# Kernel optimization log

Measured on AMD Instinct MI355X. Metric: run time of the kernel, lower is better.

The kernel has to match this reference:

```python
import jax, jax.numpy as jnp
import numpy as np

B, P, K, H = 8, 4096, 20, 128  # graphs, points per graph, kNN, hidden_channels


def _linear_init(key, fin, fout):
    s = 1.0 / np.sqrt(fin)
    kw, kb = jax.random.split(key)
    W = jax.random.uniform(kw, (fin, fout), jnp.float32, -s, s)
    b = jax.random.uniform(kb, (fout,), jnp.float32, -s, s)
    return W, b


def setup_inputs() -> dict:
    key = jax.random.key(0)
    ks = jax.random.split(key, 6)
    x = jax.random.normal(ks[0], (B, P, 3), jnp.float32)
    W1, b1 = _linear_init(ks[1], 2 * 3, H)
    W2, b2 = _linear_init(ks[2], 2 * H, H)
    W3, b3 = _linear_init(ks[3], 2 * H, H)
    W4, b4 = _linear_init(ks[4], H, H)
    W5, b5 = _linear_init(ks[5], H, 3)
    return dict(x=x, W1=W1, b1=b1, W2=W2, b2=b2, W3=W3, b3=b3,
                W4=W4, b4=b4, W5=W5, b5=b5)


def _dynamic_edge_conv(x, W, b):
    # x: [B, P, D]. Recompute kNN graph in feature space, EdgeConv with max aggr.
    sq = jnp.sum(x * x, axis=-1)                                   # [B, P]
    d2 = sq[:, :, None] + sq[:, None, :] - 2.0 * jnp.einsum('bid,bjd->bij', x, x)
    eye = jnp.eye(x.shape[1], dtype=bool)                          # exclude self-loops
    d2 = jnp.where(eye[None], jnp.inf, d2)
    _, idx = jax.lax.top_k(-d2, K)                                 # [B, P, K]
    xj = jax.vmap(lambda xb, ib: xb[ib])(x, idx)                   # [B, P, K, D] gather
    xi = jnp.broadcast_to(x[:, :, None, :], xj.shape)
    e = jnp.concatenate([xi, xj - xi], axis=-1)                    # [B, P, K, 2D]
    h = jax.nn.relu(e @ W + b)                                     # edge MLP
    return jnp.max(h, axis=2)                                      # max aggregation -> [B, P, H]


def reference(x, W1, b1, W2, b2, W3, b3, W4, b4, W5, b5):
    h = jax.nn.relu(_dynamic_edge_conv(x, W1, b1))
    h = jax.nn.relu(_dynamic_edge_conv(h, W2, b2))
    h = jax.nn.relu(_dynamic_edge_conv(h, W3, b3))
    g = jnp.mean(h, axis=1)                                        # global_mean_pool -> [B, H]
    g = jax.nn.relu(g @ W4 + b4)
    # dropout is identity in eval mode
    return g @ W5 + b5                                             # [B, 3]
```

## Files before the change

kernel.cpp:

```cpp
#include <hip/hip_runtime.h>
#include <hip/hip_bf16.h>


static constexpr int B_ = 8, P_ = 4096, K_ = 20, H_ = 128;
static constexpr float FINF = 3.0e38f;
static constexpr int CAPH = 160;

typedef __attribute__((ext_vector_type(8))) short short8;
typedef __attribute__((ext_vector_type(16))) float floatx16;

__device__ __forceinline__ float dist3(float x0, float x1, float x2,
                                       const float4& v) {
  return fmaf(-2.f, fmaf(x0, v.x, fmaf(x1, v.y, x2 * v.z)), v.w);
}

__global__ __launch_bounds__(256) void pack4_kernel(const float* __restrict__ X,
                                                    float4* __restrict__ pt4) {
  int p = blockIdx.x * 256 + threadIdx.x;
  const float* row = X + (size_t)p * 3;
  float4 v;
  v.x = row[0]; v.y = row[1]; v.z = row[2];
  v.w = fmaf(v.x, v.x, fmaf(v.y, v.y, v.z * v.z));
  pt4[p] = v;
}

__global__ __launch_bounds__(256) void split_kernel(const float* __restrict__ X,
                                                    ushort* __restrict__ hi,
                                                    ushort* __restrict__ lo,
                                                    float* __restrict__ sqn) {
  int t = blockIdx.x * 256 + threadIdx.x;
  int gp = t >> 4;
  int q = t & 15;
  const float* src = X + ((size_t)gp << 7) + (q << 3);
  size_t dst = ((size_t)gp << 7) + ((size_t)(q ^ (gp & 15)) << 3);
  float4 v0 = *(const float4*)src;
  float4 v1 = *(const float4*)(src + 4);
  float vv[8] = {v0.x, v0.y, v0.z, v0.w, v1.x, v1.y, v1.z, v1.w};
  ushort h[8], l[8];
  float ss = 0.f;
#pragma unroll
  for (int e = 0; e < 8; ++e) {
    ss = fmaf(vv[e], vv[e], ss);
    __hip_bfloat16 hb = __float2bfloat16(vv[e]);
    float hf = __bfloat162float(hb);
    __hip_bfloat16 lb = __float2bfloat16(vv[e] - hf);
    h[e] = *(ushort*)&hb;
    l[e] = *(ushort*)&lb;
  }
  *(short8*)(hi + dst) = *(short8*)h;
  *(short8*)(lo + dst) = *(short8*)l;
#pragma unroll
  for (int off = 1; off < 16; off <<= 1) ss += __shfl_xor(ss, off);
  if (q == 0) sqn[gp] = ss;
}

__global__ __launch_bounds__(256) void feat3_kernel(
    const float* __restrict__ X, const float* __restrict__ W,
    const float* __restrict__ bias, float* __restrict__ c_out,
    float* __restrict__ u_out) {
  const int h = threadIdx.x & (H_ - 1);
  const int pg = threadIdx.x >> 7;
  const int bb = blockIdx.x & 7;
  const int pb = blockIdx.x >> 3;
  const int p0 = bb * P_ + pb * 8 + pg * 4;
  float a0 = 0, a1 = 0, a2 = 0, a3 = 0, u0 = 0, u1 = 0, u2 = 0, u3 = 0;
  const float* xp = X + (size_t)p0 * 3;
#pragma unroll
  for (int d = 0; d < 3; ++d) {
    float wt = W[d * H_ + h];
    float wb = W[(3 + d) * H_ + h];
    float x0 = xp[d], x1 = xp[3 + d], x2 = xp[6 + d], x3 = xp[9 + d];
    a0 = fmaf(x0, wt, a0); u0 = fmaf(x0, wb, u0);
    a1 = fmaf(x1, wt, a1); u1 = fmaf(x1, wb, u1);
    a2 = fmaf(x2, wt, a2); u2 = fmaf(x2, wb, u2);
    a3 = fmaf(x3, wt, a3); u3 = fmaf(x3, wb, u3);
  }
  float bv = bias[h];
  c_out[(size_t)(p0 + 0) * H_ + h] = a0 - u0 + bv;
  c_out[(size_t)(p0 + 1) * H_ + h] = a1 - u1 + bv;
  c_out[(size_t)(p0 + 2) * H_ + h] = a2 - u2 + bv;
  c_out[(size_t)(p0 + 3) * H_ + h] = a3 - u3 + bv;
  u_out[(size_t)(p0 + 0) * H_ + h] = u0;
  u_out[(size_t)(p0 + 1) * H_ + h] = u1;
  u_out[(size_t)(p0 + 2) * H_ + h] = u2;
  u_out[(size_t)(p0 + 3) * H_ + h] = u3;
}

__global__ __launch_bounds__(256) void wprep_kernel(const float* __restrict__ W,
                                                    ushort* __restrict__ Vfh,
                                                    ushort* __restrict__ Vfl) {
  int tid = blockIdx.x * 256 + threadIdx.x;
  int t = tid >> 9;
  int s = (tid >> 6) & 7;
  int lane = tid & 63;
  int col = t * 32 + (lane & 31);
  int kb = s * 16 + ((lane >> 5) << 3);
  ushort h[8], l[8];
#pragma unroll
  for (int e = 0; e < 8; ++e) {
    int k = kb + e;
    float v;
    if (col < 128) v = W[k * H_ + col] - W[(128 + k) * H_ + col];
    else v = W[(128 + k) * H_ + col - 128];
    __hip_bfloat16 hb = __float2bfloat16(v);
    float hf = __bfloat162float(hb);
    __hip_bfloat16 lb = __float2bfloat16(v - hf);
    h[e] = *(ushort*)&hb;
    l[e] = *(ushort*)&lb;
  }
  size_t off = (size_t)((t * 8 + s) * 64 + lane) * 8;
  *(short8*)(Vfh + off) = *(short8*)h;
  *(short8*)(Vfl + off) = *(short8*)l;
}

__device__ __forceinline__ void stage_async(const ushort* __restrict__ Xhi,
                                            const ushort* __restrict__ Xlo,
                                            size_t tile, char* buf, int w,
                                            int lane) {
  const char* gh = (const char*)(Xhi + tile);
  const char* gl = (const char*)(Xlo + tile);
  const int lo16 = lane * 16;
#pragma unroll
  for (int it = 0; it < 4; ++it) {
    const int off = (w * 4 + it) * 1024;
    __builtin_amdgcn_global_load_lds(
        (const __attribute__((address_space(1))) void*)(gh + off + lo16),
        (__attribute__((address_space(3))) void*)(buf + off), 16, 0, 0);
    __builtin_amdgcn_global_load_lds(
        (const __attribute__((address_space(1))) void*)(gl + off + lo16),
        (__attribute__((address_space(3))) void*)(buf + 16384 + off), 16, 0, 0);
  }
}

__device__ __forceinline__ void stage_async32(const ushort* __restrict__ Xhi,
                                              const ushort* __restrict__ Xlo,
                                              size_t tile, char* buf, int w,
                                              int lane) {
  const char* gh = (const char*)(Xhi + tile);
  const char* gl = (const char*)(Xlo + tile);
  const int lo16 = lane * 16;
#pragma unroll
  for (int it = 0; it < 4; ++it) {
    const int off = (w * 4 + it) * 1024;
    __builtin_amdgcn_global_load_lds(
        (const __attribute__((address_space(1))) void*)(gh + off + lo16),
        (__attribute__((address_space(3))) void*)(buf + off), 16, 0, 0);
    __builtin_amdgcn_global_load_lds(
        (const __attribute__((address_space(1))) void*)(gl + off + lo16),
        (__attribute__((address_space(3))) void*)(buf + 8192 + off), 16, 0, 0);
  }
}

__device__ __forceinline__ void load_afrag_sw(const ushort* __restrict__ X,
                                              size_t gb, int row, int lane,
                                              short8* a) {
  const ushort* base = X + (gb + row) * (size_t)H_;
  const int x = row & 15;
  const int kh = lane >> 5;
#pragma unroll
  for (int s = 0; s < 8; ++s) {
    a[s] = *(const short8*)(base + (((s * 2 + kh) ^ x) << 3));
  }
}

__device__ __forceinline__ floatx16 gram32(const char* lds, const short8* ahi,
                                           const short8* alo, int jh,
                                           int lane) {
  floatx16 a0, a1, a2;
#pragma unroll
  for (int i = 0; i < 16; ++i) { a0[i] = 0.f; a1[i] = 0.f; a2[i] = 0.f; }
  const int base = (jh * 32 + (lane & 31)) * 256;
  const int kh = lane >> 5;
  const int x = lane & 15;
#pragma unroll
  for (int s = 0; s < 8; ++s) {
    const int off = base + (((s * 2 + kh) ^ x) << 4);
    short8 bh = *(const short8*)(lds + off);
    short8 bl = *(const short8*)(lds + 16384 + off);
    a0 = __builtin_amdgcn_mfma_f32_32x32x16_bf16(ahi[s], bh, a0, 0, 0, 0);
    a1 = __builtin_amdgcn_mfma_f32_32x32x16_bf16(ahi[s], bl, a1, 0, 0, 0);
    a2 = __builtin_amdgcn_mfma_f32_32x32x16_bf16(alo[s], bh, a2, 0, 0, 0);
  }
  floatx16 acc;
#pragma unroll
  for (int i = 0; i < 16; ++i) acc[i] = (a0[i] + a1[i]) + a2[i];
  return acc;
}

__device__ __forceinline__ floatx16 gram32t(const char* lds, const short8* ahi,
                                            const short8* alo, int lane) {
  floatx16 a0, a1, a2;
#pragma unroll
  for (int i = 0; i < 16; ++i) { a0[i] = 0.f; a1[i] = 0.f; a2[i] = 0.f; }
  const int base = (lane & 31) * 256;
  const int kh = lane >> 5;
  const int x = lane & 15;
#pragma unroll
  for (int s = 0; s < 8; ++s) {
    const int off = base + (((s * 2 + kh) ^ x) << 4);
    short8 bh = *(const short8*)(lds + off);
    short8 bl = *(const short8*)(lds + 8192 + off);
    a0 = __builtin_amdgcn_mfma_f32_32x32x16_bf16(ahi[s], bh, a0, 0, 0, 0);
    a1 = __builtin_amdgcn_mfma_f32_32x32x16_bf16(ahi[s], bl, a1, 0, 0, 0);
    a2 = __builtin_amdgcn_mfma_f32_32x32x16_bf16(alo[s], bh, a2, 0, 0, 0);
  }
  floatx16 acc;
#pragma unroll
  for (int i = 0; i < 16; ++i) acc[i] = (a0[i] + a1[i]) + a2[i];
  return acc;
}

__global__ __launch_bounds__(256) void feat_mfma_kernel(
    const ushort* __restrict__ Xhi, const ushort* __restrict__ Xlo,
    const ushort* __restrict__ Vfh, const ushort* __restrict__ Vfl,
    const float* __restrict__ bias, float* __restrict__ c_out,
    float* __restrict__ u_out) {
  const int lane = threadIdx.x & 63;
  const int w = threadIdx.x >> 6;
  const int b = blockIdx.x & 7;
  const int i0 = (blockIdx.x >> 3) * 32;
  const size_t gb = (size_t)b * P_;

  short8 ahi[8], alo[8];
  const int arow = i0 + (lane & 31);
  load_afrag_sw(Xhi, gb, arow, lane, ahi);
  load_afrag_sw(Xlo, gb, arow, lane, alo);

  const int rl = 4 * (lane >> 5);
#pragma unroll
  for (int tt = 0; tt < 2; ++tt) {
    const int t = w * 2 + tt;
    floatx16 a0, a1, a2;
#pragma unroll
    for (int i = 0; i < 16; ++i) { a0[i] = 0.f; a1[i] = 0.f; a2[i] = 0.f; }
#pragma unroll
    for (int s = 0; s < 8; ++s) {
      const size_t off = (size_t)((t * 8 + s) * 64 + lane) * 8;
      short8 bh = *(const short8*)(Vfh + off);
      short8 bl = *(const short8*)(Vfl + off);
      a0 = __builtin_amdgcn_mfma_f32_32x32x16_bf16(ahi[s], bh, a0, 0, 0, 0);
      a1 = __builtin_amdgcn_mfma_f32_32x32x16_bf16(ahi[s], bl, a1, 0, 0, 0);
      a2 = __builtin_amdgcn_mfma_f32_32x32x16_bf16(alo[s], bh, a2, 0, 0, 0);
    }
    const int col = t * 32 + (lane & 31);
    if (t < 4) {
      float bv = bias[col];
#pragma unroll
      for (int g = 0; g < 16; ++g) {
        int row = i0 + rl + (g & 3) + 8 * (g >> 2);
        c_out[(gb + row) * (size_t)H_ + col] = ((a0[g] + a1[g]) + a2[g]) + bv;
      }
    } else {
#pragma unroll
      for (int g = 0; g < 16; ++g) {
        int row = i0 + rl + (g & 3) + 8 * (g >> 2);
        u_out[(gb + row) * (size_t)H_ + col - 128] = (a0[g] + a1[g]) + a2[g];
      }
    }
  }
}

__device__ __forceinline__ float kth20_of32(float* v) {
  float m = 0.f;
  for (int sel = 0; sel < K_; ++sel) {
    m = v[0];
#pragma unroll
    for (int t = 1; t < 32; ++t) m = fminf(m, v[t]);
    bool done = false;
#pragma unroll
    for (int t = 0; t < 32; ++t) {
      if (!done && v[t] == m) { v[t] = FINF; done = true; }
    }
  }
  return m;
}

__global__ __launch_bounds__(256) void knn_part_kernel(
    const ushort* __restrict__ Xhi, const ushort* __restrict__ Xlo,
    const float* __restrict__ sqn, float* __restrict__ tau) {
  __shared__ char buf[32768];
  __shared__ float ldist[64 * 65];

  const int tid = threadIdx.x;
  const int lane = tid & 63;
  const int w = tid >> 6;
  const int rh = w >> 1, jh = w & 1;
  const int b = blockIdx.x & 7;
  const int i0 = (blockIdx.x >> 3) * 64;
  const size_t gb = (size_t)b * P_;

  short8 ahi[8], alo[8];
  const int arow = i0 + rh * 32 + (lane & 31);
  load_afrag_sw(Xhi, gb, arow, lane, ahi);
  load_afrag_sw(Xlo, gb, arow, lane, alo);
  const int rowb = rh * 32 + 4 * (lane >> 5);
  const int jcol = jh * 32 + (lane & 31);

  const int srow = tid >> 2;
  const int sr = tid & 3;
  const int gi = i0 + srow;
  float bd[8];
#pragma unroll
  for (int k = 0; k < 8; ++k) bd[k] = FINF;
  float worst = FINF;

  for (int ch = 0; ch < 8; ++ch) {
    const int tb = ch * 64;
    stage_async(Xhi, Xlo, (gb + tb) * (size_t)H_, buf, w, lane);
    float sqv = sqn[gb + tb + jcol];
    __syncthreads();
    floatx16 acc = gram32(buf, ahi, alo, jh, lane);
#pragma unroll
    for (int g = 0; g < 16; ++g) {
      ldist[(rowb + (g & 3) + 8 * (g >> 2)) * 65 + jcol] =
          fmaf(-2.f, acc[g], sqv);
    }
    __syncthreads();
    const float* drow = ldist + srow * 65 + sr * 16;
#pragma unroll 4
    for (int jj = 0; jj < 16; ++jj) {
      float s = drow[jj];
      int jg = tb + sr * 16 + jj;
      if (s < worst && jg != gi) {
        bool done = false;
#pragma unroll
        for (int k = 0; k < 8; ++k) {
          if (!done && bd[k] == worst) { bd[k] = s; done = true; }
        }
        worst = bd[0];
#pragma unroll
        for (int k = 1; k < 8; ++k) worst = fmaxf(worst, bd[k]);
      }
    }
  }
  __syncthreads();
#pragma unroll
  for (int k = 0; k < 8; ++k) ldist[srow * 65 + sr * 8 + k] = bd[k];
  __syncthreads();
  if (sr == 0) {
    float v[32];
#pragma unroll
    for (int t = 0; t < 32; ++t) v[t] = ldist[srow * 65 + t];
    tau[gb + gi] = kth20_of32(v);
  }
}

__global__ __launch_bounds__(128) void knn_compact_kernel(
    const ushort* __restrict__ Xhi, const ushort* __restrict__ Xlo,
    const float* __restrict__ sqn, const float* __restrict__ tau,
    float2* __restrict__ cand, int* __restrict__ cnt) {
  __shared__ char buf[2][16384];

  const int tid = threadIdx.x;
  const int lane = tid & 63;
  const int w = tid >> 6;
  const int b = blockIdx.x & 7;
  const int rest = blockIdx.x >> 3;
  const int half = rest & 1;
  const int i0 = (rest >> 1) * 64;
  const size_t gb = (size_t)b * P_;

  short8 ahi[8], alo[8];
  const int arow = i0 + w * 32 + (lane & 31);
  load_afrag_sw(Xhi, gb, arow, lane, ahi);
  load_afrag_sw(Xlo, gb, arow, lane, alo);

  const int rowb = i0 + w * 32 + 4 * (lane >> 5);
  float taur[16];
  int cur[16];
#pragma unroll
  for (int g = 0; g < 16; ++g) {
    taur[g] = tau[gb + rowb + (g & 3) + 8 * (g >> 2)];
    cur[g] = 0;
  }
  float2* candrow = cand + (gb + rowb) * (size_t)(2 * CAPH) + half * CAPH;
  const unsigned lmask = (1u << (lane & 31)) - 1u;
  const int jbase = half * 2048;

  stage_async32(Xhi, Xlo, (gb + jbase) * (size_t)H_, buf[0], w, lane);
  float sqv_next = sqn[gb + jbase + (lane & 31)];

  for (int c = 0; c < 64; ++c) {
    const int tb = jbase + c * 32;
    __syncthreads();
    float sqv = sqv_next;
    if (c < 63) {
      stage_async32(Xhi, Xlo, (gb + tb + 32) * (size_t)H_, buf[(c + 1) & 1], w,
                    lane);
      sqv_next = sqn[gb + tb + 32 + (lane & 31)];
    }
    floatx16 acc = gram32t(buf[c & 1], ahi, alo, lane);
    const int jg = tb + (lane & 31);
#pragma unroll
    for (int g = 0; g < 16; ++g) {
      float d = fmaf(-2.f, acc[g], sqv);
      bool pred = (d <= taur[g]);
      unsigned long long mk = __ballot(pred);
      if (mk) {
        unsigned seg = (lane >= 32) ? (unsigned)(mk >> 32) : (unsigned)mk;
        int idx = cur[g] + __popc(seg & lmask);
        if (pred && idx < CAPH) {
          float2 e;
          e.x = d;
          e.y = __int_as_float(jg);
          candrow[(size_t)((g & 3) + 8 * (g >> 2)) * (2 * CAPH) + idx] = e;
        }
        cur[g] += __popc(seg);
      }
    }
  }
  if ((lane & 31) == 0) {
#pragma unroll
    for (int g = 0; g < 16; ++g) {
      int row = rowb + (g & 3) + 8 * (g >> 2);
      cnt[(gb + row) * 2 + half] = cur[g] < CAPH ? cur[g] : CAPH;
    }
  }
}

__global__ __launch_bounds__(256) void knn3_part_kernel(
    const float4* __restrict__ pt4, float* __restrict__ tau) {
  __shared__ float lv[64 * 33];
  const int tid = threadIdx.x;
  const int row_local = tid >> 2;
  const int r = tid & 3;
  const int b = blockIdx.x & 7;
  const int i0 = (blockIdx.x >> 3) * 64;
  const int gi = i0 + row_local;
  const size_t gb = (size_t)b * P_;

  float4 pi = pt4[gb + gi];
  float bd[8];
#pragma unroll
  for (int k = 0; k < 8; ++k) bd[k] = FINF;
  float worst = FINF;

  const float4* pg = pt4 + gb + r * 256;
#pragma unroll 4
  for (int jj = 0; jj < 256; ++jj) {
    float4 v = pg[jj];
    float d = dist3(pi.x, pi.y, pi.z, v);
    int jg = r * 256 + jj;
    if (d < worst && jg != gi) {
      bool done = false;
#pragma unroll
      for (int k = 0; k < 8; ++k) {
        if (!done && bd[k] == worst) { bd[k] = d; done = true; }
      }
      worst = bd[0];
#pragma unroll
      for (int k = 1; k < 8; ++k) worst = fmaxf(worst, bd[k]);
    }
  }
#pragma unroll
  for (int k = 0; k < 8; ++k) lv[row_local * 33 + r * 8 + k] = bd[k];
  __syncthreads();
  if (r == 0) {
    float v[32];
#pragma unroll
    for (int t = 0; t < 32; ++t) v[t] = lv[row_local * 33 + t];
    tau[gb + gi] = kth20_of32(v);
  }
}

__global__ __launch_bounds__(256) void knn3_compact_kernel(
    const float4* __restrict__ pt4, const float* __restrict__ tau,
    float2* __restrict__ cand, int* __restrict__ cnt) {
  const int tid = threadIdx.x;
  const int lane = tid & 63;
  const int w = tid >> 6;
  const int b = blockIdx.x & 7;
  const int rest = blockIdx.x >> 3;
  const int half = rest & 1;
  const int i0 = (rest >> 1) * 64;
  const size_t gb = (size_t)b * P_;
  const int r0 = i0 + w * 16;

  float xr0[16], xr1[16], xr2[16], taur[16];
  int cur[16];
#pragma unroll
  for (int r = 0; r < 16; ++r) {
    float4 p = pt4[gb + r0 + r];
    xr0[r] = p.x; xr1[r] = p.y; xr2[r] = p.z;
    taur[r] = tau[gb + r0 + r];
    cur[r] = 0;
  }

  const float4* pg = pt4 + gb + half * 2048;
  for (int ch = 0; ch < 32; ++ch) {
    float4 v = pg[ch * 64 + lane];
    int jg = half * 2048 + ch * 64 + lane;
#pragma unroll
    for (int r = 0; r < 16; ++r) {
      float d = dist3(xr0[r], xr1[r], xr2[r], v);
      bool pred = (d <= taur[r]);
      unsigned long long mk = __ballot(pred);
      if (mk) {
        int n = __popcll(mk);
        int pre = __popcll(mk & ((1ull << lane) - 1ull));
        int idx = cur[r] + pre;
        if (pred && idx < CAPH) {
          float2 e;
          e.x = d;
          e.y = __int_as_float(jg);
          cand[(gb + r0 + r) * (size_t)(2 * CAPH) + half * CAPH + idx] = e;
        }
        cur[r] += n;
      }
    }
  }
  if (lane == 0) {
#pragma unroll
    for (int r = 0; r < 16; ++r)
      cnt[(gb + r0 + r) * 2 + half] = cur[r] < CAPH ? cur[r] : CAPH;
  }
}

__global__ __launch_bounds__(256) void select_aggr_kernel(
    const float2* __restrict__ cand, const int* __restrict__ cnt,
    const float* __restrict__ c, const float* __restrict__ u,
    float* __restrict__ out) {
  __shared__ int ljs[4][24];
  const int w = threadIdx.x >> 6;
  const int lane = threadIdx.x & 63;
  const int b = blockIdx.x & 7;
  const int row = b * P_ + (blockIdx.x >> 3) * 4 + w;
  const int c0 = cnt[row * 2], c1 = cnt[row * 2 + 1];
  const int ctot = c0 + c1;
  float d[5];
  int j[5];
#pragma unroll
  for (int s = 0; s < 5; ++s) {
    int m = s * 64 + lane;
    bool valid = m < ctot;
    int addr = (m < c0) ? m : (CAPH + m - c0);
    if (!valid) addr = 0;
    float2 e = cand[(size_t)row * (2 * CAPH) + addr];
    d[s] = valid ? e.x : FINF;
    j[s] = __float_as_int(e.y);
  }
  for (int round = 0; round < K_ + 1; ++round) {
    float bm = d[0];
    int bs = 0;
#pragma unroll
    for (int s = 1; s < 5; ++s) {
      if (d[s] < bm) { bm = d[s]; bs = s; }
    }
    int id = (lane << 3) | bs;
#pragma unroll
    for (int off = 1; off < 64; off <<= 1) {
      float od = __shfl_xor(bm, off);
      int oid = __shfl_xor(id, off);
      if (od < bm || (od == bm && oid < id)) { bm = od; id = oid; }
    }
    int owner = id >> 3, os = id & 7;
    if (lane == owner) {
      int jv = 0;
#pragma unroll
      for (int s = 0; s < 5; ++s) {
        if (s == os) { jv = j[s]; d[s] = FINF; }
      }
      ljs[w][round] = jv;
    }
  }
  const float2* c2p = (const float2*)(c + (size_t)row * H_);
  float2 ci = c2p[lane];
  float mx = 0.f, my = 0.f;
#pragma unroll 4
  for (int k = 1; k <= K_; ++k) {
    int jj = ljs[w][k];
    float2 uv = *(const float2*)(u + ((size_t)(b << 12) + jj) * H_ + lane * 2);
    mx = fmaxf(mx, ci.x + uv.x);
    my = fmaxf(my, ci.y + uv.y);
  }
  float2 o;
  o.x = mx; o.y = my;
  *(float2*)(out + (size_t)row * H_ + lane * 2) = o;
}

__global__ __launch_bounds__(128) void pool_kernel(const float* __restrict__ hf,
                                                   float* __restrict__ psum) {
  constexpr int CHUNK = 64;
  int blk = blockIdx.x;
  int b = blk >> 6;
  int chunk = blk & 63;
  int h = threadIdx.x;
  int base = (b << 12) + chunk * CHUNK;
  float acc = 0.f;
#pragma unroll 4
  for (int p = 0; p < CHUNK; ++p) acc += hf[(size_t)(base + p) * H_ + h];
  psum[blk * H_ + h] = acc;
}

__global__ __launch_bounds__(128) void head_kernel(
    const float* __restrict__ psum, const float* __restrict__ W4,
    const float* __restrict__ b4, const float* __restrict__ W5,
    const float* __restrict__ b5, float* __restrict__ out) {
  int b = blockIdx.x, h = threadIdx.x;
  __shared__ float g[H_];
  __shared__ float t[H_];
  float s = 0.f;
#pragma unroll 4
  for (int ch = 0; ch < 64; ++ch) s += psum[(b * 64 + ch) * H_ + h];
  g[h] = s * (1.0f / P_);
  __syncthreads();
  float acc = b4[h];
#pragma unroll 4
  for (int d = 0; d < H_; ++d) acc = fmaf(g[d], W4[d * H_ + h], acc);
  t[h] = fmaxf(acc, 0.f);
  __syncthreads();
  if (h < 3) {
    float o = b5[h];
#pragma unroll 4
    for (int d = 0; d < H_; ++d) o = fmaf(t[d], W5[d * 3 + h], o);
    out[b * 3 + h] = o;
  }
}

extern "C" void kernel_launch(void* const* d_in, const int* in_sizes, int n_in,
                              void* d_out, int out_size, void* d_ws,
                              size_t ws_size, hipStream_t stream) {
  const float* x  = (const float*)d_in[0];
  const float* W1 = (const float*)d_in[1];
  const float* b1 = (const float*)d_in[2];
  const float* W2 = (const float*)d_in[3];
  const float* b2 = (const float*)d_in[4];
  const float* W3 = (const float*)d_in[5];
  const float* b3 = (const float*)d_in[6];
  const float* W4 = (const float*)d_in[7];
  const float* b4 = (const float*)d_in[8];
  const float* W5 = (const float*)d_in[9];
  const float* b5 = (const float*)d_in[10];
  float* out = (float*)d_out;

  char* ws = (char*)d_ws;
  const size_t NF = (size_t)B_ * P_ * H_;
  const size_t NP_ = (size_t)B_ * P_;
  float*  bufA = (float*)ws;  ws += NF * 4;
  float*  bufB = (float*)ws;  ws += NF * 4;
  float*  bufU = (float*)ws;  ws += NF * 4;
  ushort* xhi  = (ushort*)ws; ws += NF * 2;
  ushort* xlo  = (ushort*)ws; ws += NF * 2;
  float*  sqn  = (float*)ws;  ws += NP_ * 4;
  float*  psum = (float*)ws;  ws += (size_t)B_ * 64 * H_ * 4;
  float*  tau  = (float*)ws;  ws += NP_ * 4;
  int*    cnt  = (int*)ws;    ws += NP_ * 2 * 4;
  float4* pt4  = (float4*)ws; ws += NP_ * 16;
  ushort* vfh  = (ushort*)ws; ws += 32768 * 2;
  ushort* vfl  = (ushort*)ws; ws += 32768 * 2;
  float2* cand = (float2*)ws; ws += NP_ * (size_t)(2 * CAPH) * 8;

  const int NP = B_ * P_;
  dim3 blk256(256), blk128(128);

  pack4_kernel<<<NP / 256, blk256, 0, stream>>>(x, pt4);
  feat3_kernel<<<NP / 8, blk256, 0, stream>>>(x, W1, b1, bufA, bufU);
  knn3_part_kernel<<<B_ * 64, blk256, 0, stream>>>(pt4, tau);
  knn3_compact_kernel<<<B_ * 64 * 2, blk256, 0, stream>>>(pt4, tau, cand, cnt);
  select_aggr_kernel<<<NP / 4, blk256, 0, stream>>>(cand, cnt, bufA, bufU, bufA);

  split_kernel<<<(int)(NF / 8 / 256), blk256, 0, stream>>>(bufA, xhi, xlo, sqn);
  wprep_kernel<<<16, blk256, 0, stream>>>(W2, vfh, vfl);
  feat_mfma_kernel<<<NP / 32, blk256, 0, stream>>>(xhi, xlo, vfh, vfl, b2, bufB, bufU);
  knn_part_kernel<<<B_ * 64, blk256, 0, stream>>>(xhi, xlo, sqn, tau);
  knn_compact_kernel<<<B_ * 64 * 2, blk128, 0, stream>>>(xhi, xlo, sqn, tau, cand, cnt);
  select_aggr_kernel<<<NP / 4, blk256, 0, stream>>>(cand, cnt, bufB, bufU, bufB);

  split_kernel<<<(int)(NF / 8 / 256), blk256, 0, stream>>>(bufB, xhi, xlo, sqn);
  wprep_kernel<<<16, blk256, 0, stream>>>(W3, vfh, vfl);
  feat_mfma_kernel<<<NP / 32, blk256, 0, stream>>>(xhi, xlo, vfh, vfl, b3, bufA, bufU);
  knn_part_kernel<<<B_ * 64, blk256, 0, stream>>>(xhi, xlo, sqn, tau);
  knn_compact_kernel<<<B_ * 64 * 2, blk128, 0, stream>>>(xhi, xlo, sqn, tau, cand, cnt);
  select_aggr_kernel<<<NP / 4, blk256, 0, stream>>>(cand, cnt, bufA, bufU, bufA);

  pool_kernel<<<B_ * 64, blk128, 0, stream>>>(bufA, psum);
  head_kernel<<<B_, blk128, 0, stream>>>(psum, W4, b4, W5, b5, out);
}
```

Baseline: 1.104 ms.

## Fuse kernels across layers to cut launches and intermediate traffic

Merges several stages into fewer kernels. pack4 moves into the first feature kernel, the two wprep launches become one, and the layer-1 kNN part and compact steps become one kernel with tau kept in LDS. The bf16 hi/lo split and squared norms move into the aggregation epilogue, and the MFMA feature GEMM moves into the kNN-part kernel, which now handles 64 rows per block. This removes kernel launches and a full read and write of the fp32 activations per layer. In exchange, the fused kNN kernel recomputes the partial top-k in each of its two halves, and the feature GEMM now runs on fewer, larger blocks.

```diff
diff --git a/kernel.cpp b/kernel.cpp
--- a/kernel.cpp
+++ b/kernel.cpp
@@ -14,55 +14,31 @@
   return fmaf(-2.f, fmaf(x0, v.x, fmaf(x1, v.y, x2 * v.z)), v.w);
 }
 
-__global__ __launch_bounds__(256) void pack4_kernel(const float* __restrict__ X,
-                                                    float4* __restrict__ pt4) {
-  int p = blockIdx.x * 256 + threadIdx.x;
-  const float* row = X + (size_t)p * 3;
-  float4 v;
-  v.x = row[0]; v.y = row[1]; v.z = row[2];
-  v.w = fmaf(v.x, v.x, fmaf(v.y, v.y, v.z * v.z));
-  pt4[p] = v;
-}
-
-__global__ __launch_bounds__(256) void split_kernel(const float* __restrict__ X,
-                                                    ushort* __restrict__ hi,
-                                                    ushort* __restrict__ lo,
-                                                    float* __restrict__ sqn) {
-  int t = blockIdx.x * 256 + threadIdx.x;
-  int gp = t >> 4;
-  int q = t & 15;
-  const float* src = X + ((size_t)gp << 7) + (q << 3);
-  size_t dst = ((size_t)gp << 7) + ((size_t)(q ^ (gp & 15)) << 3);
-  float4 v0 = *(const float4*)src;
-  float4 v1 = *(const float4*)(src + 4);
-  float vv[8] = {v0.x, v0.y, v0.z, v0.w, v1.x, v1.y, v1.z, v1.w};
-  ushort h[8], l[8];
-  float ss = 0.f;
-#pragma unroll
-  for (int e = 0; e < 8; ++e) {
-    ss = fmaf(vv[e], vv[e], ss);
-    __hip_bfloat16 hb = __float2bfloat16(vv[e]);
-    float hf = __bfloat162float(hb);
-    __hip_bfloat16 lb = __float2bfloat16(vv[e] - hf);
-    h[e] = *(ushort*)&hb;
-    l[e] = *(ushort*)&lb;
-  }
-  *(short8*)(hi + dst) = *(short8*)h;
-  *(short8*)(lo + dst) = *(short8*)l;
-#pragma unroll
-  for (int off = 1; off < 16; off <<= 1) ss += __shfl_xor(ss, off);
-  if (q == 0) sqn[gp] = ss;
-}
-
-__global__ __launch_bounds__(256) void feat3_kernel(
+__device__ __forceinline__ void cvt_split(float v, ushort& h, ushort& l) {
+  __hip_bfloat16 hb = __float2bfloat16(v);
+  float hf = __bfloat162float(hb);
+  __hip_bfloat16 lb = __float2bfloat16(v - hf);
+  h = *(ushort*)&hb;
+  l = *(ushort*)&lb;
+}
+
+__global__ __launch_bounds__(256) void feat3p_kernel(
     const float* __restrict__ X, const float* __restrict__ W,
     const float* __restrict__ bias, float* __restrict__ c_out,
-    float* __restrict__ u_out) {
+    float* __restrict__ u_out, float4* __restrict__ pt4) {
   const int h = threadIdx.x & (H_ - 1);
   const int pg = threadIdx.x >> 7;
   const int bb = blockIdx.x & 7;
   const int pb = blockIdx.x >> 3;
-  const int p0 = bb * P_ + pb * 8 + pg * 4;
+  const int pbase = bb * P_ + pb * 8;
+  const int p0 = pbase + pg * 4;
+  if (threadIdx.x < 8) {
+    const float* row = X + (size_t)(pbase + threadIdx.x) * 3;
+    float4 v;
+    v.x = row[0]; v.y = row[1]; v.z = row[2];
+    v.w = fmaf(v.x, v.x, fmaf(v.y, v.y, v.z * v.z));
+    pt4[pbase + threadIdx.x] = v;
+  }
   float a0 = 0, a1 = 0, a2 = 0, a3 = 0, u0 = 0, u1 = 0, u2 = 0, u3 = 0;
   const float* xp = X + (size_t)p0 * 3;
 #pragma unroll
@@ -86,10 +62,15 @@
   u_out[(size_t)(p0 + 3) * H_ + h] = u3;
 }
 
-__global__ __launch_bounds__(256) void wprep_kernel(const float* __restrict__ W,
-                                                    ushort* __restrict__ Vfh,
-                                                    ushort* __restrict__ Vfl) {
-  int tid = blockIdx.x * 256 + threadIdx.x;
+__global__ __launch_bounds__(256) void wprep2_kernel(
+    const float* __restrict__ W2, const float* __restrict__ W3,
+    ushort* __restrict__ Vfh2, ushort* __restrict__ Vfl2,
+    ushort* __restrict__ Vfh3, ushort* __restrict__ Vfl3) {
+  const int which = blockIdx.x >> 4;
+  const float* W = which ? W3 : W2;
+  ushort* Vfh = which ? Vfh3 : Vfh2;
+  ushort* Vfl = which ? Vfl3 : Vfl2;
+  int tid = (blockIdx.x & 15) * 256 + threadIdx.x;
   int t = tid >> 9;
   int s = (tid >> 6) & 7;
   int lane = tid & 63;
@@ -102,11 +83,7 @@
     float v;
     if (col < 128) v = W[k * H_ + col] - W[(128 + k) * H_ + col];
     else v = W[(128 + k) * H_ + col - 128];
-    __hip_bfloat16 hb = __float2bfloat16(v);
-    float hf = __bfloat162float(hb);
-    __hip_bfloat16 lb = __float2bfloat16(v - hf);
-    h[e] = *(ushort*)&hb;
-    l[e] = *(ushort*)&lb;
+    cvt_split(v, h[e], l[e]);
   }
   size_t off = (size_t)((t * 8 + s) * 64 + lane) * 8;
   *(short8*)(Vfh + off) = *(short8*)h;
@@ -210,26 +187,47 @@
   return acc;
 }
 
-__global__ __launch_bounds__(256) void feat_mfma_kernel(
+__device__ __forceinline__ float kth20_of32(float* v) {
+  float m = 0.f;
+  for (int sel = 0; sel < K_; ++sel) {
+    m = v[0];
+#pragma unroll
+    for (int t = 1; t < 32; ++t) m = fminf(m, v[t]);
+    bool done = false;
+#pragma unroll
+    for (int t = 0; t < 32; ++t) {
+      if (!done && v[t] == m) { v[t] = FINF; done = true; }
+    }
+  }
+  return m;
+}
+
+__global__ __launch_bounds__(256) void featpart_kernel(
     const ushort* __restrict__ Xhi, const ushort* __restrict__ Xlo,
     const ushort* __restrict__ Vfh, const ushort* __restrict__ Vfl,
     const float* __restrict__ bias, float* __restrict__ c_out,
-    float* __restrict__ u_out) {
-  const int lane = threadIdx.x & 63;
-  const int w = threadIdx.x >> 6;
+    float* __restrict__ u_out, const float* __restrict__ sqn,
+    float* __restrict__ tau) {
+  __shared__ char buf[32768];
+  __shared__ float ldist[64 * 65];
+
+  const int tid = threadIdx.x;
+  const int lane = tid & 63;
+  const int w = tid >> 6;
+  const int rh = w >> 1, jh = w & 1;
   const int b = blockIdx.x & 7;
-  const int i0 = (blockIdx.x >> 3) * 32;
+  const int i0 = (blockIdx.x >> 3) * 64;
   const size_t gb = (size_t)b * P_;
 
   short8 ahi[8], alo[8];
-  const int arow = i0 + (lane & 31);
+  const int arow = i0 + rh * 32 + (lane & 31);
   load_afrag_sw(Xhi, gb, arow, lane, ahi);
   load_afrag_sw(Xlo, gb, arow, lane, alo);
 
   const int rl = 4 * (lane >> 5);
 #pragma unroll
-  for (int tt = 0; tt < 2; ++tt) {
-    const int t = w * 2 + tt;
+  for (int tt = 0; tt < 4; ++tt) {
+    const int t = jh * 4 + tt;
     floatx16 a0, a1, a2;
 #pragma unroll
     for (int i = 0; i < 16; ++i) { a0[i] = 0.f; a1[i] = 0.f; a2[i] = 0.f; }
@@ -243,59 +241,24 @@
       a2 = __builtin_amdgcn_mfma_f32_32x32x16_bf16(alo[s], bh, a2, 0, 0, 0);
     }
     const int col = t * 32 + (lane & 31);
-    if (t < 4) {
+    if (jh == 0) {
       float bv = bias[col];
 #pragma unroll
       for (int g = 0; g < 16; ++g) {
-        int row = i0 + rl + (g & 3) + 8 * (g >> 2);
+        int row = i0 + rh * 32 + rl + (g & 3) + 8 * (g >> 2);
         c_out[(gb + row) * (size_t)H_ + col] = ((a0[g] + a1[g]) + a2[g]) + bv;
       }
     } else {
 #pragma unroll
       for (int g = 0; g < 16; ++g) {
-        int row = i0 + rl + (g & 3) + 8 * (g >> 2);
+        int row = i0 + rh * 32 + rl + (g & 3) + 8 * (g >> 2);
         u_out[(gb + row) * (size_t)H_ + col - 128] = (a0[g] + a1[g]) + a2[g];
       }
     }
   }
-}
-
-__device__ __forceinline__ float kth20_of32(float* v) {
-  float m = 0.f;
-  for (int sel = 0; sel < K_; ++sel) {
-    m = v[0];
-#pragma unroll
-    for (int t = 1; t < 32; ++t) m = fminf(m, v[t]);
-    bool done = false;
-#pragma unroll
-    for (int t = 0; t < 32; ++t) {
-      if (!done && v[t] == m) { v[t] = FINF; done = true; }
-    }
-  }
-  return m;
-}
-
-__global__ __launch_bounds__(256) void knn_part_kernel(
-    const ushort* __restrict__ Xhi, const ushort* __restrict__ Xlo,
-    const float* __restrict__ sqn, float* __restrict__ tau) {
-  __shared__ char buf[32768];
-  __shared__ float ldist[64 * 65];
-
-  const int tid = threadIdx.x;
-  const int lane = tid & 63;
-  const int w = tid >> 6;
-  const int rh = w >> 1, jh = w & 1;
-  const int b = blockIdx.x & 7;
-  const int i0 = (blockIdx.x >> 3) * 64;
-  const size_t gb = (size_t)b * P_;
-
-  short8 ahi[8], alo[8];
-  const int arow = i0 + rh * 32 + (lane & 31);
-  load_afrag_sw(Xhi, gb, arow, lane, ahi);
-  load_afrag_sw(Xlo, gb, arow, lane, alo);
-  const int rowb = rh * 32 + 4 * (lane >> 5);
+
+  const int rowb = rh * 32 + rl;
   const int jcol = jh * 32 + (lane & 31);
-
   const int srow = tid >> 2;
   const int sr = tid & 3;
   const int gi = i0 + srow;
@@ -418,74 +381,68 @@
   }
 }
 
-__global__ __launch_bounds__(256) void knn3_part_kernel(
-    const float4* __restrict__ pt4, float* __restrict__ tau) {
+__global__ __launch_bounds__(256) void knn3_full_kernel(
+    const float4* __restrict__ pt4, float2* __restrict__ cand,
+    int* __restrict__ cnt) {
   __shared__ float lv[64 * 33];
+  __shared__ float ltau[64];
   const int tid = threadIdx.x;
-  const int row_local = tid >> 2;
-  const int r = tid & 3;
-  const int b = blockIdx.x & 7;
-  const int i0 = (blockIdx.x >> 3) * 64;
-  const int gi = i0 + row_local;
-  const size_t gb = (size_t)b * P_;
-
-  float4 pi = pt4[gb + gi];
-  float bd[8];
-#pragma unroll
-  for (int k = 0; k < 8; ++k) bd[k] = FINF;
-  float worst = FINF;
-
-  const float4* pg = pt4 + gb + r * 256;
-#pragma unroll 4
-  for (int jj = 0; jj < 256; ++jj) {
-    float4 v = pg[jj];
-    float d = dist3(pi.x, pi.y, pi.z, v);
-    int jg = r * 256 + jj;
-    if (d < worst && jg != gi) {
-      bool done = false;
-#pragma unroll
-      for (int k = 0; k < 8; ++k) {
-        if (!done && bd[k] == worst) { bd[k] = d; done = true; }
-      }
-      worst = bd[0];
-#pragma unroll
-      for (int k = 1; k < 8; ++k) worst = fmaxf(worst, bd[k]);
-    }
-  }
-#pragma unroll
-  for (int k = 0; k < 8; ++k) lv[row_local * 33 + r * 8 + k] = bd[k];
-  __syncthreads();
-  if (r == 0) {
-    float v[32];
-#pragma unroll
-    for (int t = 0; t < 32; ++t) v[t] = lv[row_local * 33 + t];
-    tau[gb + gi] = kth20_of32(v);
-  }
-}
-
-__global__ __launch_bounds__(256) void knn3_compact_kernel(
-    const float4* __restrict__ pt4, const float* __restrict__ tau,
-    float2* __restrict__ cand, int* __restrict__ cnt) {
-  const int tid = threadIdx.x;
-  const int lane = tid & 63;
-  const int w = tid >> 6;
   const int b = blockIdx.x & 7;
   const int rest = blockIdx.x >> 3;
   const int half = rest & 1;
   const int i0 = (rest >> 1) * 64;
   const size_t gb = (size_t)b * P_;
+
+  {
+    const int row_local = tid >> 2;
+    const int r = tid & 3;
+    const int gi = i0 + row_local;
+    float4 pi = pt4[gb + gi];
+    float bd[8];
+#pragma unroll
+    for (int k = 0; k < 8; ++k) bd[k] = FINF;
+    float worst = FINF;
+    const float4* pg = pt4 + gb + r * 256;
+#pragma unroll 4
+    for (int jj = 0; jj < 256; ++jj) {
+      float4 v = pg[jj];
+      float d = dist3(pi.x, pi.y, pi.z, v);
+      int jg = r * 256 + jj;
+      if (d < worst && jg != gi) {
+        bool done = false;
+#pragma unroll
+        for (int k = 0; k < 8; ++k) {
+          if (!done && bd[k] == worst) { bd[k] = d; done = true; }
+        }
+        worst = bd[0];
+#pragma unroll
+        for (int k = 1; k < 8; ++k) worst = fmaxf(worst, bd[k]);
+      }
+    }
+#pragma unroll
+    for (int k = 0; k < 8; ++k) lv[row_local * 33 + r * 8 + k] = bd[k];
+    __syncthreads();
+    if (r == 0) {
+      float v[32];
+#pragma unroll
+      for (int t = 0; t < 32; ++t) v[t] = lv[row_local * 33 + t];
+      ltau[row_local] = kth20_of32(v);
+    }
+  }
+  __syncthreads();
+
+  const int lane = tid & 63;
+  const int w = tid >> 6;
   const int r0 = i0 + w * 16;
-
   float xr0[16], xr1[16], xr2[16], taur[16];
   int cur[16];
 #pragma unroll
   for (int r = 0; r < 16; ++r) {
     float4 p = pt4[gb + r0 + r];
     xr0[r] = p.x; xr1[r] = p.y; xr2[r] = p.z;
-    taur[r] = tau[gb + r0 + r];
+    taur[r] = ltau[w * 16 + r];
     cur[r] = 0;
   }
-
   const float4* pg = pt4 + gb + half * 2048;
   for (int ch = 0; ch < 32; ++ch) {
     float4 v = pg[ch * 64 + lane];
@@ -516,15 +473,18 @@
   }
 }
 
-__global__ __launch_bounds__(256) void select_aggr_kernel(
+__global__ __launch_bounds__(256) void selsplit_kernel(
     const float2* __restrict__ cand, const int* __restrict__ cnt,
     const float* __restrict__ c, const float* __restrict__ u,
-    float* __restrict__ out) {
+    float* __restrict__ out, ushort* __restrict__ hi,
+    ushort* __restrict__ lo, float* __restrict__ sqn) {
   __shared__ int ljs[4][24];
+  __shared__ float aggv[4][128];
   const int w = threadIdx.x >> 6;
   const int lane = threadIdx.x & 63;
   const int b = blockIdx.x & 7;
-  const int row = b * P_ + (blockIdx.x >> 3) * 4 + w;
+  const int rowbase = b * P_ + (blockIdx.x >> 3) * 4;
+  const int row = rowbase + w;
   const int c0 = cnt[row * 2], c1 = cnt[row * 2 + 1];
   const int ctot = c0 + c1;
   float d[5];
@@ -573,9 +533,36 @@
     mx = fmaxf(mx, ci.x + uv.x);
     my = fmaxf(my, ci.y + uv.y);
   }
-  float2 o;
-  o.x = mx; o.y = my;
-  *(float2*)(out + (size_t)row * H_ + lane * 2) = o;
+  if (out != nullptr) {
+    float2 o;
+    o.x = mx; o.y = my;
+    *(float2*)(out + (size_t)row * H_ + lane * 2) = o;
+  }
+  if (hi != nullptr) {
+    aggv[w][lane * 2] = mx;
+    aggv[w][lane * 2 + 1] = my;
+    __syncthreads();
+    const int tid = threadIdx.x;
+    if (tid < 64) {
+      const int r = tid >> 4, m = tid & 15;
+      const int rrow = rowbase + r;
+      float vv[8];
+      float ss = 0.f;
+      ushort hh[8], ll[8];
+#pragma unroll
+      for (int e = 0; e < 8; ++e) {
+        vv[e] = aggv[r][m * 8 + e];
+        ss = fmaf(vv[e], vv[e], ss);
+        cvt_split(vv[e], hh[e], ll[e]);
+      }
+      size_t dst = ((size_t)rrow << 7) + ((size_t)(m ^ (rrow & 15)) << 3);
+      *(short8*)(hi + dst) = *(short8*)hh;
+      *(short8*)(lo + dst) = *(short8*)ll;
+#pragma unroll
+      for (int off = 1; off < 16; off <<= 1) ss += __shfl_xor(ss, off);
+      if (m == 0) sqn[rrow] = ss;
+    }
+  }
 }
 
 __global__ __launch_bounds__(128) void pool_kernel(const float* __restrict__ hf,
@@ -646,32 +633,36 @@
   float*  tau  = (float*)ws;  ws += NP_ * 4;
   int*    cnt  = (int*)ws;    ws += NP_ * 2 * 4;
   float4* pt4  = (float4*)ws; ws += NP_ * 16;
-  ushort* vfh  = (ushort*)ws; ws += 32768 * 2;
-  ushort* vfl  = (ushort*)ws; ws += 32768 * 2;
+  ushort* vfh2 = (ushort*)ws; ws += 32768 * 2;
+  ushort* vfl2 = (ushort*)ws; ws += 32768 * 2;
+  ushort* vfh3 = (ushort*)ws; ws += 32768 * 2;
+  ushort* vfl3 = (ushort*)ws; ws += 32768 * 2;
   float2* cand = (float2*)ws; ws += NP_ * (size_t)(2 * CAPH) * 8;
 
   const int NP = B_ * P_;
   dim3 blk256(256), blk128(128);
 
-  pack4_kernel<<<NP / 256, blk256, 0, stream>>>(x, pt4);
-  feat3_kernel<<<NP / 8, blk256, 0, stream>>>(x, W1, b1, bufA, bufU);
-  knn3_part_kernel<<<B_ * 64, blk256, 0, stream>>>(pt4, tau);
-  knn3_compact_kernel<<<B_ * 64 * 2, blk256, 0, stream>>>(pt4, tau, cand, cnt);
-  select_aggr_kernel<<<NP / 4, blk256, 0, stream>>>(cand, cnt, bufA, bufU, bufA);
-
-  split_kernel<<<(int)(NF / 8 / 256), blk256, 0, stream>>>(bufA, xhi, xlo, sqn);
-  wprep_kernel<<<16, blk256, 0, stream>>>(W2, vfh, vfl);
-  feat_mfma_kernel<<<NP / 32, blk256, 0, stream>>>(xhi, xlo, vfh, vfl, b2, bufB, bufU);
-  knn_part_kernel<<<B_ * 64, blk256, 0, stream>>>(xhi, xlo, sqn, tau);
-  knn_compact_kernel<<<B_ * 64 * 2, blk128, 0, stream>>>(xhi, xlo, sqn, tau, cand, cnt);
-  select_aggr_kernel<<<NP / 4, blk256, 0, stream>>>(cand, cnt, bufB, bufU, bufB);
-
-  split_kernel<<<(int)(NF / 8 / 256), blk256, 0, stream>>>(bufB, xhi, xlo, sqn);
-  wprep_kernel<<<16, blk256, 0, stream>>>(W3, vfh, vfl);
-  feat_mfma_kernel<<<NP / 32, blk256, 0, stream>>>(xhi, xlo, vfh, vfl, b3, bufA, bufU);
-  knn_part_kernel<<<B_ * 64, blk256, 0, stream>>>(xhi, xlo, sqn, tau);
-  knn_compact_kernel<<<B_ * 64 * 2, blk128, 0, stream>>>(xhi, xlo, sqn, tau, cand, cnt);
-  select_aggr_kernel<<<NP / 4, blk256, 0, stream>>>(cand, cnt, bufA, bufU, bufA);
+  wprep2_kernel<<<32, blk256, 0, stream>>>(W2, W3, vfh2, vfl2, vfh3, vfl3);
+
+  feat3p_kernel<<<NP / 8, blk256, 0, stream>>>(x, W1, b1, bufA, bufU, pt4);
+  knn3_full_kernel<<<B_ * 64 * 2, blk256, 0, stream>>>(pt4, cand, cnt);
+  selsplit_kernel<<<NP / 4, blk256, 0, stream>>>(cand, cnt, bufA, bufU,
+                                                 nullptr, xhi, xlo, sqn);
+
+  featpart_kernel<<<B_ * 64, blk256, 0, stream>>>(xhi, xlo, vfh2, vfl2, b2,
+                                                  bufB, bufU, sqn, tau);
+  knn_compact_kernel<<<B_ * 64 * 2, blk128, 0, stream>>>(xhi, xlo, sqn, tau,
+                                                         cand, cnt);
+  selsplit_kernel<<<NP / 4, blk256, 0, stream>>>(cand, cnt, bufB, bufU,
+                                                 nullptr, xhi, xlo, sqn);
+
+  featpart_kernel<<<B_ * 64, blk256, 0, stream>>>(xhi, xlo, vfh3, vfl3, b3,
+                                                  bufB, bufU, sqn, tau);
+  knn_compact_kernel<<<B_ * 64 * 2, blk128, 0, stream>>>(xhi, xlo, sqn, tau,
+                                                         cand, cnt);
+  selsplit_kernel<<<NP / 4, blk256, 0, stream>>>(cand, cnt, bufB, bufU,
+                                                 bufA, nullptr, nullptr,
+                                                 nullptr);
 
   pool_kernel<<<B_ * 64, blk128, 0, stream>>>(bufA, psum);
   head_kernel<<<B_, blk128, 0, stream>>>(psum, W4, b4, W5, b5, out);
```

New measurement: 1.179 ms. +6.8%, slower.
